# Kernel optimization log

Hardware: AMD Instinct MI355X
Metric: run time of the kernel (lower is better)

## Reference

```python
import jax, jax.numpy as jnp
import numpy as np

# FlowNetC correlation config (kernel_size=1 -> pointwise patch; pad == max_displacement)
PAD = 20
MAX_DISP = 20
STRIDE2 = 2


def setup_inputs() -> dict:
    key = jax.random.key(0)
    k1, k2 = jax.random.split(key)
    B, C, H, W = 4, 256, 96, 96
    input1 = jax.random.normal(k1, (B, C, H, W), dtype=jnp.float32)
    input2 = jax.random.normal(k2, (B, C, H, W), dtype=jnp.float32)
    return {"input1": input1, "input2": input2}


def _correlation(x1, x2):
    # x1, x2: [B, C, H, W]. Output: [B, D*D, H, W] with D = 2*MAX_DISP//STRIDE2 + 1.
    B, C, H, W = x1.shape
    x2p = jnp.pad(x2, ((0, 0), (0, 0), (PAD, PAD), (PAD, PAD)))
    D = 2 * MAX_DISP // STRIDE2 + 1  # 21
    # start index into padded map = PAD + (disp) where disp = off - MAX_DISP;
    # since PAD == MAX_DISP, start index == off.
    offs = jnp.arange(D, dtype=jnp.int32) * STRIDE2
    dyv, dxv = jnp.meshgrid(offs, offs, indexing="ij")
    pairs = jnp.stack([dyv.ravel(), dxv.ravel()], axis=1)  # [D*D, 2]
    inv_c = jnp.float32(1.0 / C)  # CUDA kernel divides by kernel^2 * C (kernel=1)

    def body(_, p):
        dy, dx = p[0], p[1]
        sl = jax.lax.dynamic_slice(x2p, (0, 0, dy, dx), (B, C, H, W))
        return None, jnp.einsum("bchw,bchw->bhw", x1, sl) * inv_c

    _, corr = jax.lax.scan(body, None, pairs)  # [D*D, B, H, W]
    return corr.transpose(1, 0, 2, 3)  # [B, D*D, H, W]


def reference(input1, input2):
    return _correlation(input1, input2)
```

## Files before the change

### kernel.cpp

```cpp
#include <hip/hip_runtime.h>
#include <hip/hip_bf16.h>


typedef __bf16 bf16x8 __attribute__((ext_vector_type(8)));
typedef float f32x4 __attribute__((ext_vector_type(4)));

#define B_ 4
#define C_ 256
#define H_ 96
#define W_ 96
#define NOFF 21
#define ROWS 96
#define IMG_ELEMS (ROWS * C_)
#define X1T_ELEMS (B_ * H_ * IMG_ELEMS)

__device__ __forceinline__ unsigned short f32_to_bf16_rne(float f) {
    union { float f; unsigned u; } v; v.f = f;
    unsigned u = v.u;
    return (unsigned short)((u + 0x7fffu + ((u >> 16) & 1u)) >> 16);
}

__device__ __forceinline__ void gl2lds16(const void* g, void* l) {
    __builtin_amdgcn_global_load_lds(
        (const __attribute__((address_space(1))) void*)g,
        (__attribute__((address_space(3))) void*)l, 16, 0, 0);
}

__global__ __launch_bounds__(256) void prep_kernel(const float* __restrict__ x1,
                                                   const float* __restrict__ x2,
                                                   unsigned short* __restrict__ ws) {
    __shared__ float tile[96 * 65];
    int bid = blockIdx.x;
    int cblk  = bid & 3;
    int which = (bid >> 2) & 1;
    int bh    = bid >> 3;
    int h = bh % H_;
    int b = bh / H_;
    int c0 = cblk << 6;

    const float* src = (which ? x2 : x1) + ((size_t)(b * C_ + c0) * H_ + h) * W_;
    unsigned short* dst = ws + (size_t)which * X1T_ELEMS + (size_t)(b * H_ + h) * IMG_ELEMS;

    for (int idx = threadIdx.x; idx < 64 * 96; idx += 256) {
        int c = idx / 96, w = idx - c * 96;
        tile[w * 65 + c] = src[c * (H_ * W_) + w];
    }
    __syncthreads();

    for (int idx = threadIdx.x; idx < 96 * 8; idx += 256) {
        int row = idx >> 3, tp = idx & 7;
        int par = row / 48, i = row - par * 48;
        int w = 2 * i + par;
        int s = tp ^ (row & 7);
        const float* fsrc = &tile[w * 65 + (s << 3)];
        unsigned pk[4];
#pragma unroll
        for (int e = 0; e < 4; ++e) {
            unsigned lo = f32_to_bf16_rne(fsrc[2 * e]);
            unsigned hi = f32_to_bf16_rne(fsrc[2 * e + 1]);
            pk[e] = lo | (hi << 16);
        }
        int ccp = (((c0 >> 3) ^ (row & 24)) + tp);
        *(uint4*)((char*)(dst + (size_t)row * C_) + (ccp << 4)) =
            make_uint4(pk[0], pk[1], pk[2], pk[3]);
    }
}

__global__ __launch_bounds__(384, 3) void corr_kernel(const unsigned short* __restrict__ ws,
                                                      float* __restrict__ out) {
    __shared__ unsigned short Bs[IMG_ELEMS];
    __shared__ float sl[NOFF][97];

    int bid = blockIdx.x;
    int xcd = bid & 7, sidx = bid >> 3;
    int b  = xcd >> 1;
    int h  = ((xcd & 1) ? 48 : 0) + (sidx >> 1);
    int og = sidx & 1;

    int tid = threadIdx.x;
    int wv = tid >> 6, lane = tid & 63;
    int par = wv & 1, mt = wv >> 1;
    int i0 = mt << 4;
    int n = lane & 15, quad = lane >> 4;

    int rowA = par * 48 + i0 + n;
    const unsigned short* Ag = ws + (size_t)(b * H_ + h) * IMG_ELEMS + (size_t)rowA * C_;
    int keyA = rowA & 31;
    bf16x8 afrag[8];
#pragma unroll
    for (int ks = 0; ks < 8; ++ks)
        afrag[ks] = *(const bf16x8*)(Ag + ((((ks << 2) | quad) ^ keyA) << 3));

    const unsigned short* Bimg = ws + (size_t)X1T_ELEMS + (size_t)(b * H_) * IMG_ELEMS;

    int rowB0 = par * 48 + n;
    int rowB1 = rowB0 + 16;
    int rowB2 = rowB0 + 32;
    int keyB0 = rowB0 & 31, keyB1 = rowB1 & 31, keyB2 = rowB2 & 31;

    int oy_lo = og ? 11 : 0;
    int oy_hi = og ? NOFF : 11;
    int wvoff  = wv * 8192;
    int gmaoff = wvoff + lane * 16;

    for (int oy = oy_lo; oy < oy_hi; ++oy) {
        int h2 = h + 2 * oy - 20;
        int outb = ((b * 441 + oy * NOFF) * H_ + h) * W_;
        if (h2 < 0 || h2 >= H_) {
            for (int idx = tid; idx < NOFF * W_; idx += 384)
                out[outb + (idx / W_) * (H_ * W_) + (idx % W_)] = 0.0f;
            continue;
        }

        const char* Bg = (const char*)(Bimg + (size_t)h2 * IMG_ELEMS);
#pragma unroll
        for (int c = 0; c < 8; ++c)
            gl2lds16(Bg + gmaoff + c * 1024, (char*)Bs + wvoff + c * 1024);
        __syncthreads();

        f32x4 acc0 = {0.f,0.f,0.f,0.f}, acc1 = {0.f,0.f,0.f,0.f}, acc2 = {0.f,0.f,0.f,0.f};
        const char* Bsb = (const char*)Bs;
        if (mt == 0) {
#pragma unroll
            for (int ks = 0; ks < 8; ++ks) {
                int ci = (ks << 2) | quad;
                bf16x8 b0 = *(const bf16x8*)(Bsb + rowB0 * 512 + ((ci ^ keyB0) << 4));
                bf16x8 b1 = *(const bf16x8*)(Bsb + rowB1 * 512 + ((ci ^ keyB1) << 4));
                acc0 = __builtin_amdgcn_mfma_f32_16x16x32_bf16(afrag[ks], b0, acc0, 0, 0, 0);
                acc1 = __builtin_amdgcn_mfma_f32_16x16x32_bf16(afrag[ks], b1, acc1, 0, 0, 0);
            }
        } else if (mt == 1) {
#pragma unroll
            for (int ks = 0; ks < 8; ++ks) {
                int ci = (ks << 2) | quad;
                bf16x8 b0 = *(const bf16x8*)(Bsb + rowB0 * 512 + ((ci ^ keyB0) << 4));
                bf16x8 b1 = *(const bf16x8*)(Bsb + rowB1 * 512 + ((ci ^ keyB1) << 4));
                bf16x8 b2 = *(const bf16x8*)(Bsb + rowB2 * 512 + ((ci ^ keyB2) << 4));
                acc0 = __builtin_amdgcn_mfma_f32_16x16x32_bf16(afrag[ks], b0, acc0, 0, 0, 0);
                acc1 = __builtin_amdgcn_mfma_f32_16x16x32_bf16(afrag[ks], b1, acc1, 0, 0, 0);
                acc2 = __builtin_amdgcn_mfma_f32_16x16x32_bf16(afrag[ks], b2, acc2, 0, 0, 0);
            }
        } else {
#pragma unroll
            for (int ks = 0; ks < 8; ++ks) {
                int ci = (ks << 2) | quad;
                bf16x8 b1 = *(const bf16x8*)(Bsb + rowB1 * 512 + ((ci ^ keyB1) << 4));
                bf16x8 b2 = *(const bf16x8*)(Bsb + rowB2 * 512 + ((ci ^ keyB2) << 4));
                acc1 = __builtin_amdgcn_mfma_f32_16x16x32_bf16(afrag[ks], b1, acc1, 0, 0, 0);
                acc2 = __builtin_amdgcn_mfma_f32_16x16x32_bf16(afrag[ks], b2, acc2, 0, 0, 0);
            }
        }

#pragma unroll
        for (int r = 0; r < 4; ++r) {
            int m = (quad << 2) + r;
            int w = 2 * (i0 + m) + par;
            int oxb = n - i0 - m - 6;
            if (mt != 2) { int ox = 16 + oxb; if (ox >= 0 && ox < NOFF) sl[ox][w] = acc0[r]; }
            {             int ox = 32 + oxb; if (ox >= 0 && ox < NOFF) sl[ox][w] = acc1[r]; }
            if (mt != 0) { int ox = 48 + oxb; if (ox >= 0 && ox < NOFF) sl[ox][w] = acc2[r]; }
        }
        __syncthreads();

        for (int idx = tid; idx < NOFF * W_; idx += 384) {
            int ox = idx / W_, w = idx - ox * W_;
            int w2 = w + 2 * ox - 20;
            float v = (w2 >= 0 && w2 < W_) ? sl[ox][w] * (1.0f / 256.0f) : 0.0f;
            out[outb + ox * (H_ * W_) + w] = v;
        }
    }
}

__global__ __launch_bounds__(256) void corr_fallback(const float* __restrict__ x1,
                                                     const float* __restrict__ x2,
                                                     float* __restrict__ out) {
    int bid = blockIdx.x;
    int oy = bid % NOFF, h = (bid / NOFF) % H_, b = bid / (NOFF * H_);
    int dy = 2 * oy - 20, h2 = h + dy;
    int outbase = ((b * 441 + oy * NOFF) * H_ + h) * W_;
    for (int idx = threadIdx.x; idx < NOFF * W_; idx += 256) {
        int ox = idx / W_, w = idx % W_;
        float acc = 0.f;
        int w2 = w + 2 * ox - 20;
        if (h2 >= 0 && h2 < H_ && w2 >= 0 && w2 < W_) {
            const float* p1 = x1 + (size_t)b * C_ * H_ * W_ + h * W_ + w;
            const float* p2 = x2 + (size_t)b * C_ * H_ * W_ + h2 * W_ + w2;
            for (int c = 0; c < C_; ++c) acc += p1[c * (H_ * W_)] * p2[c * (H_ * W_)];
        }
        out[outbase + ox * (H_ * W_) + w] = acc * (1.0f / 256.0f);
    }
}

extern "C" void kernel_launch(void* const* d_in, const int* in_sizes, int n_in,
                              void* d_out, int out_size, void* d_ws, size_t ws_size,
                              hipStream_t stream) {
    const float* x1 = (const float*)d_in[0];
    const float* x2 = (const float*)d_in[1];
    float* out = (float*)d_out;

    size_t need = (size_t)2 * X1T_ELEMS * sizeof(unsigned short);
    if (ws_size >= need) {
        unsigned short* ws = (unsigned short*)d_ws;
        prep_kernel<<<B_ * H_ * 2 * 4, 256, 0, stream>>>(x1, x2, ws);
        corr_kernel<<<768, 384, 0, stream>>>(ws, out);
    } else {
        corr_fallback<<<B_ * H_ * NOFF, 256, 0, stream>>>(x1, x2, out);
    }
}
```

Before: 179.0 us.

## Restructure correlation kernel to load B fragments directly from global, per-wave slab output

Drops the LDS staging of the x2 row and the block-wide barriers. Each wave now loads its B fragment straight from global memory into registers, holds up to two A tiles, and writes results into a private per-wave LDS slab using precomputed store masks. The grid is split more finely: per (b,h) there are 3 oy groups of 7 and 2 parities, giving 2304 blocks of 256 threads. The prep kernel's XOR swizzle is removed because LDS bank conflicts for B no longer matter. In exchange, B loads from global are repeated across blocks with no LDS reuse, and out-of-range rows now compute and store zeros rather than skipping the compute.

Result: slower. 193.8 us (+8.3%).

```diff
diff --git a/kernel.cpp b/kernel.cpp
--- a/kernel.cpp
+++ b/kernel.cpp
@@ -10,20 +10,13 @@
 #define H_ 96
 #define W_ 96
 #define NOFF 21
-#define ROWS 96
-#define IMG_ELEMS (ROWS * C_)
+#define IMG_ELEMS (96 * C_)
 #define X1T_ELEMS (B_ * H_ * IMG_ELEMS)
 
 __device__ __forceinline__ unsigned short f32_to_bf16_rne(float f) {
     union { float f; unsigned u; } v; v.f = f;
     unsigned u = v.u;
     return (unsigned short)((u + 0x7fffu + ((u >> 16) & 1u)) >> 16);
-}
-
-__device__ __forceinline__ void gl2lds16(const void* g, void* l) {
-    __builtin_amdgcn_global_load_lds(
-        (const __attribute__((address_space(1))) void*)g,
-        (__attribute__((address_space(3))) void*)l, 16, 0, 0);
 }
 
 __global__ __launch_bounds__(256) void prep_kernel(const float* __restrict__ x1,
@@ -51,8 +44,7 @@
         int row = idx >> 3, tp = idx & 7;
         int par = row / 48, i = row - par * 48;
         int w = 2 * i + par;
-        int s = tp ^ (row & 7);
-        const float* fsrc = &tile[w * 65 + (s << 3)];
+        const float* fsrc = &tile[w * 65 + (tp << 3)];
         unsigned pk[4];
 #pragma unroll
         for (int e = 0; e < 4; ++e) {
@@ -60,113 +52,117 @@
             unsigned hi = f32_to_bf16_rne(fsrc[2 * e + 1]);
             pk[e] = lo | (hi << 16);
         }
-        int ccp = (((c0 >> 3) ^ (row & 24)) + tp);
-        *(uint4*)((char*)(dst + (size_t)row * C_) + (ccp << 4)) =
+        *(uint4*)(dst + (size_t)row * C_ + c0 + (tp << 3)) =
             make_uint4(pk[0], pk[1], pk[2], pk[3]);
     }
 }
 
-__global__ __launch_bounds__(384, 3) void corr_kernel(const unsigned short* __restrict__ ws,
+__global__ __launch_bounds__(256, 3) void corr_kernel(const unsigned short* __restrict__ ws,
                                                       float* __restrict__ out) {
-    __shared__ unsigned short Bs[IMG_ELEMS];
-    __shared__ float sl[NOFF][97];
+    __shared__ float slab[3264];
 
     int bid = blockIdx.x;
-    int xcd = bid & 7, sidx = bid >> 3;
+    int xcd = bid & 7, rest = bid >> 3;
     int b  = xcd >> 1;
-    int h  = ((xcd & 1) ? 48 : 0) + (sidx >> 1);
-    int og = sidx & 1;
+    int h  = ((xcd & 1) ? 48 : 0) + rest / 6;
+    int sub = rest % 6;
+    int og = sub >> 1, par = sub & 1;
 
     int tid = threadIdx.x;
     int wv = tid >> 6, lane = tid & 63;
-    int par = wv & 1, mt = wv >> 1;
-    int i0 = mt << 4;
-    int n = lane & 15, quad = lane >> 4;
-
-    int rowA = par * 48 + i0 + n;
-    const unsigned short* Ag = ws + (size_t)(b * H_ + h) * IMG_ELEMS + (size_t)rowA * C_;
-    int keyA = rowA & 31;
-    bf16x8 afrag[8];
-#pragma unroll
-    for (int ks = 0; ks < 8; ++ks)
-        afrag[ks] = *(const bf16x8*)(Ag + ((((ks << 2) | quad) ^ keyA) << 3));
-
-    const unsigned short* Bimg = ws + (size_t)X1T_ELEMS + (size_t)(b * H_) * IMG_ELEMS;
-
-    int rowB0 = par * 48 + n;
-    int rowB1 = rowB0 + 16;
-    int rowB2 = rowB0 + 32;
-    int keyB0 = rowB0 & 31, keyB1 = rowB1 & 31, keyB2 = rowB2 & 31;
-
-    int oy_lo = og ? 11 : 0;
-    int oy_hi = og ? NOFF : 11;
-    int wvoff  = wv * 8192;
-    int gmaoff = wvoff + lane * 16;
-
-    for (int oy = oy_lo; oy < oy_hi; ++oy) {
+    int n = lane & 15, q = lane >> 4;
+
+    const int utab[4]  = {0, 1, 1, 2};
+    const int mtbt[4]  = {0, 0, 2, 1};
+    const int nmtt[4]  = {2, 2, 1, 2};
+    int u = utab[wv], mtb = mtbt[wv], nmt = nmtt[wv];
+
+    const unsigned short* ws1 = ws;
+    const unsigned short* ws2 = ws + X1T_ELEMS;
+
+    bf16x8 afrag[2][8];
+#pragma unroll
+    for (int mtl = 0; mtl < 2; ++mtl) {
+        if (mtl < nmt) {
+            int rowA = par * 48 + 16 * (mtb + mtl) + n;
+            const unsigned short* Ab = ws1 + (size_t)(b * H_ + h) * IMG_ELEMS
+                                           + rowA * C_ + q * 8;
+#pragma unroll
+            for (int ks = 0; ks < 8; ++ks)
+                afrag[mtl][ks] = *(const bf16x8*)(Ab + ks * 32);
+        }
+    }
+
+    int rowB = par * 48 + 16 * u + n;
+    const unsigned short* Bbase0 = ws2 + (size_t)(b * H_) * IMG_ELEMS + rowB * C_ + q * 8;
+
+    int ox00 = 16 * u - 16 * mtb + n - 4 * q + 10;
+    int scb2 = wv * 800 + 19 * ox00 + 4 * q;
+
+    int ek[11];
+#pragma unroll
+    for (int k = 0; k < 11; ++k) {
+        int f = k * 64 + lane;
+        int m = f & 15, g = f >> 4;
+        int mtl = (g >= 21) ? 1 : 0;
+        int ox = g - 21 * mtl;
+        int live = (f < nmt * 336) && (mtl < nmt) && (ox < 21);
+        int i = 16 * (mtb + mtl) + m;
+        int j = i + ox - 10;
+        int uo = (j < 0) ? 0 : ((j >= 48) ? 2 : (j >> 4));
+        int e = ox * 9216 + 2 * i + par;
+        if (j >= 0 && j < 48) e |= 0x40000000;
+        if (live && uo == u)  e |= 0x80000000u;
+        ek[k] = e;
+    }
+    int sb = wv * 800 + lane + 3 * (lane >> 4);
+
+    int oy0 = og * 7;
+    float* op0 = out + (size_t)((b * 441 + oy0 * NOFF) * H_ + h) * W_;
+
+    for (int t = 0; t < 7; ++t) {
+        int oy = oy0 + t;
         int h2 = h + 2 * oy - 20;
-        int outb = ((b * 441 + oy * NOFF) * H_ + h) * W_;
-        if (h2 < 0 || h2 >= H_) {
-            for (int idx = tid; idx < NOFF * W_; idx += 384)
-                out[outb + (idx / W_) * (H_ * W_) + (idx % W_)] = 0.0f;
-            continue;
-        }
-
-        const char* Bg = (const char*)(Bimg + (size_t)h2 * IMG_ELEMS);
-#pragma unroll
-        for (int c = 0; c < 8; ++c)
-            gl2lds16(Bg + gmaoff + c * 1024, (char*)Bs + wvoff + c * 1024);
-        __syncthreads();
-
-        f32x4 acc0 = {0.f,0.f,0.f,0.f}, acc1 = {0.f,0.f,0.f,0.f}, acc2 = {0.f,0.f,0.f,0.f};
-        const char* Bsb = (const char*)Bs;
-        if (mt == 0) {
+        int valid = ((unsigned)h2 < 96u);
+        int h2c = valid ? h2 : 0;
+        float scalef = valid ? (1.0f / 256.0f) : 0.0f;
+
+        const unsigned short* Bb = Bbase0 + (size_t)h2c * IMG_ELEMS;
+        bf16x8 bf[8];
+#pragma unroll
+        for (int ks = 0; ks < 8; ++ks)
+            bf[ks] = *(const bf16x8*)(Bb + ks * 32);
+
+        f32x4 acc0 = {0.f, 0.f, 0.f, 0.f};
+        f32x4 acc1 = {0.f, 0.f, 0.f, 0.f};
+        if (nmt > 1) {
 #pragma unroll
             for (int ks = 0; ks < 8; ++ks) {
-                int ci = (ks << 2) | quad;
-                bf16x8 b0 = *(const bf16x8*)(Bsb + rowB0 * 512 + ((ci ^ keyB0) << 4));
-                bf16x8 b1 = *(const bf16x8*)(Bsb + rowB1 * 512 + ((ci ^ keyB1) << 4));
-                acc0 = __builtin_amdgcn_mfma_f32_16x16x32_bf16(afrag[ks], b0, acc0, 0, 0, 0);
-                acc1 = __builtin_amdgcn_mfma_f32_16x16x32_bf16(afrag[ks], b1, acc1, 0, 0, 0);
-            }
-        } else if (mt == 1) {
-#pragma unroll
-            for (int ks = 0; ks < 8; ++ks) {
-                int ci = (ks << 2) | quad;
-                bf16x8 b0 = *(const bf16x8*)(Bsb + rowB0 * 512 + ((ci ^ keyB0) << 4));
-                bf16x8 b1 = *(const bf16x8*)(Bsb + rowB1 * 512 + ((ci ^ keyB1) << 4));
-                bf16x8 b2 = *(const bf16x8*)(Bsb + rowB2 * 512 + ((ci ^ keyB2) << 4));
-                acc0 = __builtin_amdgcn_mfma_f32_16x16x32_bf16(afrag[ks], b0, acc0, 0, 0, 0);
-                acc1 = __builtin_amdgcn_mfma_f32_16x16x32_bf16(afrag[ks], b1, acc1, 0, 0, 0);
-                acc2 = __builtin_amdgcn_mfma_f32_16x16x32_bf16(afrag[ks], b2, acc2, 0, 0, 0);
+                acc0 = __builtin_amdgcn_mfma_f32_16x16x32_bf16(afrag[0][ks], bf[ks], acc0, 0, 0, 0);
+                acc1 = __builtin_amdgcn_mfma_f32_16x16x32_bf16(afrag[1][ks], bf[ks], acc1, 0, 0, 0);
             }
         } else {
 #pragma unroll
-            for (int ks = 0; ks < 8; ++ks) {
-                int ci = (ks << 2) | quad;
-                bf16x8 b1 = *(const bf16x8*)(Bsb + rowB1 * 512 + ((ci ^ keyB1) << 4));
-                bf16x8 b2 = *(const bf16x8*)(Bsb + rowB2 * 512 + ((ci ^ keyB2) << 4));
-                acc1 = __builtin_amdgcn_mfma_f32_16x16x32_bf16(afrag[ks], b1, acc1, 0, 0, 0);
-                acc2 = __builtin_amdgcn_mfma_f32_16x16x32_bf16(afrag[ks], b2, acc2, 0, 0, 0);
-            }
+            for (int ks = 0; ks < 8; ++ks)
+                acc0 = __builtin_amdgcn_mfma_f32_16x16x32_bf16(afrag[0][ks], bf[ks], acc0, 0, 0, 0);
         }
 
 #pragma unroll
         for (int r = 0; r < 4; ++r) {
-            int m = (quad << 2) + r;
-            int w = 2 * (i0 + m) + par;
-            int oxb = n - i0 - m - 6;
-            if (mt != 2) { int ox = 16 + oxb; if (ox >= 0 && ox < NOFF) sl[ox][w] = acc0[r]; }
-            {             int ox = 32 + oxb; if (ox >= 0 && ox < NOFF) sl[ox][w] = acc1[r]; }
-            if (mt != 0) { int ox = 48 + oxb; if (ox >= 0 && ox < NOFF) sl[ox][w] = acc2[r]; }
-        }
-        __syncthreads();
-
-        for (int idx = tid; idx < NOFF * W_; idx += 384) {
-            int ox = idx / W_, w = idx - ox * W_;
-            int w2 = w + 2 * ox - 20;
-            float v = (w2 >= 0 && w2 < W_) ? sl[ox][w] * (1.0f / 256.0f) : 0.0f;
-            out[outb + ox * (H_ * W_) + w] = v;
+            if ((unsigned)(ox00 - r) < 21u)
+                slab[scb2 - 18 * r] = acc0[r];
+            if (nmt > 1 && (unsigned)(ox00 - 16 - r) < 21u)
+                slab[scb2 + 95 - 18 * r] = acc1[r];
+        }
+
+        float* op = op0 + t * (NOFF * H_ * W_);
+#pragma unroll
+        for (int k = 0; k < 11; ++k) {
+            int e = ek[k];
+            float v = slab[sb + 76 * k];
+            float val = (e & 0x40000000) ? v * scalef : 0.0f;
+            if (e < 0)
+                op[e & 0x0FFFFFFF] = val;
         }
     }
 }
@@ -202,7 +198,7 @@
     if (ws_size >= need) {
         unsigned short* ws = (unsigned short*)d_ws;
         prep_kernel<<<B_ * H_ * 2 * 4, 256, 0, stream>>>(x1, x2, ws);
-        corr_kernel<<<768, 384, 0, stream>>>(ws, out);
+        corr_kernel<<<2304, 256, 0, stream>>>(ws, out);
     } else {
         corr_fallback<<<B_ * H_ * NOFF, 256, 0, stream>>>(x1, x2, out);
     }
```
